# Kernel tuning notes

Hardware: AMD Instinct MI355X
Metric: run time of the kernel (lower is better)

The kernel has to match this reference:

```python
import jax, jax.numpy as jnp
import numpy as np

B, S, E, H = 2, 2048, 768, 12
D = E // H  # 64
ALPHA = 2.0
BANDWIDTH = 1.0
A_EXP = 0.5
RADIUS = 1.0
EPS = 1e-7
LN_EPS = 1e-12


def _l2norm(x, axis=-1):
    n = jnp.sqrt(jnp.sum(x * x, axis=axis, keepdims=True))
    return x / jnp.maximum(n, 1e-12)


def setup_inputs() -> dict:
    key = jax.random.key(0)
    ks = jax.random.split(key, 9)
    sc = 1.0 / np.sqrt(E)
    return {
        "hidden_states": jax.random.normal(ks[0], (B, S, E), dtype=jnp.float32),
        "Wq": jax.random.normal(ks[1], (E, E), dtype=jnp.float32) * sc,
        "bq": jnp.zeros((E,), dtype=jnp.float32),
        "Wk": jax.random.normal(ks[2], (E, E), dtype=jnp.float32) * sc,
        "bk": jnp.zeros((E,), dtype=jnp.float32),
        "Wv": jax.random.normal(ks[3], (E, E), dtype=jnp.float32) * sc,
        "bv": jnp.zeros((E,), dtype=jnp.float32),
        "Wo": jax.random.normal(ks[4], (E, E), dtype=jnp.float32) * sc,
        "bo": jnp.zeros((E,), dtype=jnp.float32),
        "ln_g": jnp.ones((E,), dtype=jnp.float32),
        "ln_b": jnp.zeros((E,), dtype=jnp.float32),
    }


def reference(hidden_states, Wq, bq, Wk, bk, Wv, bv, Wo, bo, ln_g, ln_b):
    # Spherical-kernel self-attention (SPFNSSelfAttention), eval mode (dropout=0)
    hs = _l2norm(hidden_states)                      # [B,S,E] embed onto sphere

    def heads(x):
        return x.reshape(B, S, H, D).transpose(0, 2, 1, 3)  # [B,H,S,D]

    q = _l2norm(heads(hs @ Wq + bq))
    k = _l2norm(heads(hs @ Wk + bk))
    v = heads(hs @ Wv + bv)

    # geodesic distance on the sphere
    cos = jnp.clip(jnp.einsum('bhsd,bhtd->bhst', q, k), -1.0 + EPS, 1.0 - EPS)
    g_dist = jnp.arccos(cos) * RADIUS                # [B,H,S,S]

    # alpha >= 2 branch: exponential kernel, exponent alpha/(alpha-1)
    p = ALPHA / (ALPHA - 1.0)
    attn_score = jnp.exp(-((g_dist / np.sqrt(BANDWIDTH)) ** p))

    # doubly-stochastic (Sinkhorn-like) scaling: diag(rowsum^-a) K diag(colsum^-a)
    row = jnp.sum(attn_score, axis=-1) ** (-A_EXP)   # [B,H,S]
    col = jnp.sum(attn_score, axis=-2) ** (-A_EXP)   # [B,H,S]
    K_tilde = attn_score * row[..., :, None] * col[..., None, :]

    # L1 row-normalize (F.normalize p=1, dim=3)
    denom = jnp.maximum(jnp.sum(jnp.abs(K_tilde), axis=-1, keepdims=True), 1e-12)
    attn_weights = K_tilde / denom

    attn_out = jnp.einsum('bhst,bhtd->bhsd', attn_weights, v)  # [B,H,S,D]
    # faithful to original: raw reshape [B,H,S,D] -> [B,S,H,D] -> [B,S,E]
    # (transpose(0,1) pair in the original cancels)
    attn_out = attn_out.reshape(B, S, E)

    # ModelSelfOutput: dense + residual(add original hidden_states) + LayerNorm
    y = attn_out @ Wo + bo + hidden_states
    mu = jnp.mean(y, axis=-1, keepdims=True)
    var = jnp.mean((y - mu) ** 2, axis=-1, keepdims=True)
    out = (y - mu) / jnp.sqrt(var + LN_EPS) * ln_g + ln_b
    return out
```

## Files before the change

kernel.cpp:

```cpp
#include <hip/hip_runtime.h>
#include <hip/hip_bf16.h>
#include <math.h>

#define BB 2
#define SS 2048
#define EE 768
#define HH 12
#define DD 64
#define MM (BB*SS)
#define BH (BB*HH)
#define NM ((size_t)MM*EE)
#define WSZ ((size_t)EE*EE)
#define BHS ((size_t)BH*SS)

typedef __attribute__((ext_vector_type(8))) short bf16x8;
typedef __attribute__((ext_vector_type(4))) float f32x4;

__device__ __forceinline__ float wave_sum64(float v) {
#pragma unroll
  for (int off = 32; off > 0; off >>= 1) v += __shfl_down(v, off, 64);
  return v;
}

__device__ __forceinline__ unsigned int pack_bf2(float x, float y) {
  unsigned int a = __float_as_uint(x), b = __float_as_uint(y);
  a += 0x7fffu + ((a >> 16) & 1u);
  b += 0x7fffu + ((b >> 16) & 1u);
  return (a >> 16) | (b & 0xffff0000u);
}
__device__ __forceinline__ unsigned int cvtpk_bf2(float x, float y) {
  __hip_bfloat162 h = __float22bfloat162_rn(make_float2(x, y));
  union { __hip_bfloat162 h2; unsigned int u; } c; c.h2 = h;
  return c.u;
}
__device__ __forceinline__ ushort bf16_1(float x) {
  unsigned int u = __float_as_uint(x);
  u += 0x7fffu + ((u >> 16) & 1u);
  return (ushort)(u >> 16);
}

__device__ __forceinline__ void score_wp(float cosv, float& w, float& p) {
  w = fmaxf(fmaf(cosv, -0.5f, 0.5f), 0.0f);
  p = fmaf(w, -0.544f, -0.2462720f);
  p = fmaf(w, p, -0.3250794f);
  p = fmaf(w, p, -0.4571429f);
  p = fmaf(w, p, -0.7111111f);
  p = fmaf(w, p, -1.3333333f);
  p = fmaf(w, p, -4.0f);
}

__global__ __launch_bounds__(256) void k_rownorm(const float* __restrict__ x,
                                                 ushort* __restrict__ o) {
  int row = blockIdx.x;
  int tid = threadIdx.x;
  const float* xr = x + (size_t)row * EE;
  ushort* orow = o + (size_t)row * EE;
  float v0 = xr[tid], v1 = xr[tid + 256], v2 = xr[tid + 512];
  float ss = v0 * v0 + v1 * v1 + v2 * v2;
  ss = wave_sum64(ss);
  __shared__ float red[4];
  if ((tid & 63) == 0) red[tid >> 6] = ss;
  __syncthreads();
  float tot = red[0] + red[1] + red[2] + red[3];
  float sc = 1.0f / fmaxf(sqrtf(tot), 1e-12f);
  orow[tid]       = bf16_1(v0 * sc);
  orow[tid + 256] = bf16_1(v1 * sc);
  orow[tid + 512] = bf16_1(v2 * sc);
}

__global__ __launch_bounds__(256) void k_transp(const float* __restrict__ Wq,
                                                const float* __restrict__ Wk,
                                                const float* __restrict__ Wv,
                                                const float* __restrict__ Wo,
                                                ushort* __restrict__ wt) {
  int z = blockIdx.z;
  const float* W = (z == 0) ? Wq : (z == 1) ? Wk : (z == 2) ? Wv : Wo;
  ushort* dst = wt + (size_t)z * WSZ;
  int n0 = blockIdx.x * 64, k0 = blockIdx.y * 64;
  __shared__ float t[64][65];
  int tid = threadIdx.x;
  int r4 = tid >> 4, c4 = (tid & 15) * 4;
#pragma unroll
  for (int i = 0; i < 4; ++i) {
    float4 v = *(const float4*)(W + (size_t)(k0 + i * 16 + r4) * EE + n0 + c4);
    t[i * 16 + r4][c4 + 0] = v.x; t[i * 16 + r4][c4 + 1] = v.y;
    t[i * 16 + r4][c4 + 2] = v.z; t[i * 16 + r4][c4 + 3] = v.w;
  }
  __syncthreads();
  int nr = tid >> 3, c8 = (tid & 7) * 8;
#pragma unroll
  for (int j = 0; j < 2; ++j) {
    int n = nr + j * 32;
    unsigned int p[4];
#pragma unroll
    for (int e = 0; e < 4; ++e)
      p[e] = pack_bf2(t[c8 + 2 * e][n], t[c8 + 2 * e + 1][n]);
    uint4 pv; pv.x = p[0]; pv.y = p[1]; pv.z = p[2]; pv.w = p[3];
    *(uint4*)(dst + (size_t)(n0 + n) * EE + k0 + c8) = pv;
  }
}

__global__ __launch_bounds__(256) void k_gemm_qkv_mfma(
    const ushort* __restrict__ hsb,
    const ushort* __restrict__ wt,
    const float* __restrict__ b0, const float* __restrict__ b1, const float* __restrict__ b2,
    ushort* __restrict__ qb, ushort* __restrict__ kb, ushort* __restrict__ vtb) {
  int bid = blockIdx.x;
  int xcd = bid & 7; int rr = bid >> 3;
  int n_idx = rr % 12; int m_in = (rr / 12) & 7; int z = rr / 96;
  int n0 = n_idx * 64; int m0 = (xcd * 8 + m_in) * 64;
  const ushort* W = wt + (size_t)z * WSZ;
  const float* bias = (z == 0) ? b0 : (z == 1) ? b1 : b2;
  __shared__ ushort As[2][64][72];
  __shared__ ushort Bs[2][64][72];
  int tid = threadIdx.x, w = tid >> 6, l = tid & 63, li = l & 15, g = l >> 4;
  int srow = tid >> 3, scol = (tid & 7) * 8;
  const ushort* Aba = hsb + (size_t)(m0 + srow) * EE + scol;
  const ushort* Wba = W + (size_t)(n0 + srow) * EE + scol;
  f32x4 acc[4];
#pragma unroll
  for (int u = 0; u < 4; ++u) acc[u] = (f32x4){0.f, 0.f, 0.f, 0.f};
  bf16x8 pA0 = *(const bf16x8*)(Aba);
  bf16x8 pA1 = *(const bf16x8*)(Aba + 32 * EE);
  bf16x8 pW0 = *(const bf16x8*)(Wba);
  bf16x8 pW1 = *(const bf16x8*)(Wba + 32 * EE);
  *(bf16x8*)&As[0][srow][scol] = pA0;
  *(bf16x8*)&As[0][srow + 32][scol] = pA1;
  *(bf16x8*)&Bs[0][srow][scol] = pW0;
  *(bf16x8*)&Bs[0][srow + 32][scol] = pW1;
  __syncthreads();
#pragma unroll
  for (int kt = 0; kt < 12; ++kt) {
    int cur = kt & 1;
    if (kt < 11) {
      int k0 = (kt + 1) * 64;
      pA0 = *(const bf16x8*)(Aba + k0);
      pA1 = *(const bf16x8*)(Aba + 32 * EE + k0);
      pW0 = *(const bf16x8*)(Wba + k0);
      pW1 = *(const bf16x8*)(Wba + 32 * EE + k0);
    }
    bf16x8 a0 = *(const bf16x8*)&As[cur][w * 16 + li][8 * g];
    bf16x8 a1 = *(const bf16x8*)&As[cur][w * 16 + li][32 + 8 * g];
#pragma unroll
    for (int u = 0; u < 4; ++u) {
      bf16x8 bb0 = *(const bf16x8*)&Bs[cur][u * 16 + li][8 * g];
      bf16x8 bb1 = *(const bf16x8*)&Bs[cur][u * 16 + li][32 + 8 * g];
      acc[u] = __builtin_amdgcn_mfma_f32_16x16x32_bf16(a0, bb0, acc[u], 0, 0, 0);
      acc[u] = __builtin_amdgcn_mfma_f32_16x16x32_bf16(a1, bb1, acc[u], 0, 0, 0);
    }
    __syncthreads();
    if (kt < 11) {
      int nxt = cur ^ 1;
      *(bf16x8*)&As[nxt][srow][scol] = pA0;
      *(bf16x8*)&As[nxt][srow + 32][scol] = pA1;
      *(bf16x8*)&Bs[nxt][srow][scol] = pW0;
      *(bf16x8*)&Bs[nxt][srow + 32][scol] = pW1;
      __syncthreads();
    }
  }
  float val[4][4];
#pragma unroll
  for (int u = 0; u < 4; ++u) {
    float bia = bias[n0 + u * 16 + li];
#pragma unroll
    for (int r = 0; r < 4; ++r) val[u][r] = acc[u][r] + bia;
  }
  if (z < 2) {
#pragma unroll
    for (int r = 0; r < 4; ++r) {
      float ss = val[0][r] * val[0][r] + val[1][r] * val[1][r] +
                 val[2][r] * val[2][r] + val[3][r] * val[3][r];
      ss += __shfl_xor(ss, 1, 64);
      ss += __shfl_xor(ss, 2, 64);
      ss += __shfl_xor(ss, 4, 64);
      ss += __shfl_xor(ss, 8, 64);
      float sc = rsqrtf(fmaxf(ss, 1e-24f));
#pragma unroll
      for (int u = 0; u < 4; ++u) val[u][r] *= sc;
    }
  }
  ushort (*tile)[72] = As[0];
#pragma unroll
  for (int u = 0; u < 4; ++u)
#pragma unroll
    for (int r = 0; r < 4; ++r) {
      int ml = w * 16 + 4 * g + r, d = u * 16 + li;
      if (z < 2) tile[ml][d] = bf16_1(val[u][r]);
      else       tile[d][ml] = bf16_1(val[u][r]);
    }
  __syncthreads();
  int h = n_idx, b_ = m0 >> 11, s0 = m0 & 2047;
  int bh = b_ * HH + h;
  int row = tid >> 2, c16 = (tid & 3) * 16;
  bf16x8 o0 = *(const bf16x8*)&tile[row][c16];
  bf16x8 o1 = *(const bf16x8*)&tile[row][c16 + 8];
  ushort* dst;
  if (z < 2) {
    dst = (z ? kb : qb) + ((size_t)bh * SS + s0 + row) * 64 + c16;
  } else {
    dst = vtb + ((size_t)bh * 64 + row) * SS + s0 + c16;
  }
  *(bf16x8*)dst = o0;
  *(bf16x8*)(dst + 8) = o1;
}

__global__ __launch_bounds__(256) void k_colsum_mfma(const ushort* __restrict__ qbf,
                                                     const ushort* __restrict__ kbf,
                                                     float* __restrict__ cs) {
  int bh = blockIdx.x, ttile = blockIdx.y, z = blockIdx.z;
  __shared__ float scs[4][4][16];
  int tid = threadIdx.x;
  int w = tid >> 6, l = tid & 63;
  int li = l & 15, g = l >> 4;
  const ushort* kb_base = kbf + ((size_t)bh * SS + ttile * 64) * 64;
  bf16x8 kb[4][2];
#pragma unroll
  for (int u = 0; u < 4; ++u)
#pragma unroll
    for (int kc = 0; kc < 2; ++kc)
      kb[u][kc] = *(const bf16x8*)(kb_base + (u * 16 + li) * 64 + kc * 32 + 8 * g);
  float cacc[4] = {0.f, 0.f, 0.f, 0.f};
  for (int it = 0; it < 16; ++it) {
    int s0 = ((z * 16 + it) * 4 + w) * 16;
    const ushort* qrow = qbf + ((size_t)bh * SS + s0 + li) * 64;
    bf16x8 qa0 = *(const bf16x8*)(qrow + 8 * g);
    bf16x8 qa1 = *(const bf16x8*)(qrow + 32 + 8 * g);
#pragma unroll
    for (int u = 0; u < 4; ++u) {
      f32x4 cf = {0.f, 0.f, 0.f, 0.f};
      cf = __builtin_amdgcn_mfma_f32_16x16x32_bf16(qa0, kb[u][0], cf, 0, 0, 0);
      cf = __builtin_amdgcn_mfma_f32_16x16x32_bf16(qa1, kb[u][1], cf, 0, 0, 0);
      float ww[4], pp[4];
#pragma unroll
      for (int r = 0; r < 4; ++r) score_wp(cf[r], ww[r], pp[r]);
      cacc[u] += __expf(ww[0] * pp[0]) + __expf(ww[1] * pp[1]) +
                 __expf(ww[2] * pp[2]) + __expf(ww[3] * pp[3]);
    }
  }
#pragma unroll
  for (int u = 0; u < 4; ++u) {
    cacc[u] += __shfl_xor(cacc[u], 16, 64);
    cacc[u] += __shfl_xor(cacc[u], 32, 64);
  }
  if (l < 16) {
#pragma unroll
    for (int u = 0; u < 4; ++u) scs[w][u][l] = cacc[u];
  }
  __syncthreads();
  if (tid < 64) {
    int t16 = tid & 15, u = tid >> 4;
    float s_ = scs[0][u][t16] + scs[1][u][t16] + scs[2][u][t16] + scs[3][u][t16];
    cs[(size_t)z * BHS + (size_t)bh * SS + ttile * 64 + u * 16 + t16] = s_;
  }
}

__global__ __launch_bounds__(256) void k_cwreduce(const float* __restrict__ cs,
                                                  float* __restrict__ lcw) {
  size_t g = (size_t)blockIdx.x * 256 + threadIdx.x;
  lcw[g] = -0.5f * __logf(cs[g] + cs[BHS + g]);
}

__global__ __launch_bounds__(256) void k_attn_mfma(const ushort* __restrict__ qbf,
                                                   const ushort* __restrict__ kbf,
                                                   const ushort* __restrict__ vtb,
                                                   const float* __restrict__ lcw,
                                                   float* __restrict__ po0,
                                                   float* __restrict__ po1,
                                                   float* __restrict__ prp) {
  int bh = blockIdx.x, stile = blockIdx.y, z = blockIdx.z;
  __shared__ __align__(16) ushort Kt[64][72];
  __shared__ __align__(16) ushort Vt[64][72];
  __shared__ __align__(16) unsigned int W_lds[4][16][36];
  int tid = threadIdx.x;
  int w = tid >> 6, l = tid & 63;
  int li = l & 15, g = l >> 4;
  int s = stile * 64 + w * 16 + li;
  const ushort* qrow = qbf + ((size_t)bh * SS + s) * 64;
  bf16x8 qb0 = *(const bf16x8*)(qrow + 8 * g);
  bf16x8 qb1 = *(const bf16x8*)(qrow + 32 + 8 * g);
  const float* cwp = lcw + (size_t)bh * SS;
  const ushort* kb_h = kbf + (size_t)bh * SS * 64;
  const ushort* vt_h = vtb + (size_t)bh * 64 * SS;
  float* po = (z == 0) ? po0 : po1;
  int sr = tid >> 3, sc = (tid & 7) * 8;
  f32x4 oacc[4];
#pragma unroll
  for (int dt = 0; dt < 4; ++dt) oacc[dt] = (f32x4){0.f, 0.f, 0.f, 0.f};
  float rp = 0.f;
  int tt0 = z * 16;
  bf16x8 rk0 = *(const bf16x8*)(kb_h + (size_t)(tt0 * 64 + sr) * 64 + sc);
  bf16x8 rk1 = *(const bf16x8*)(kb_h + (size_t)(tt0 * 64 + sr + 32) * 64 + sc);
  bf16x8 rv0 = *(const bf16x8*)(vt_h + (size_t)sr * SS + tt0 * 64 + sc);
  bf16x8 rv1 = *(const bf16x8*)(vt_h + (size_t)(sr + 32) * SS + tt0 * 64 + sc);
  for (int tt = tt0; tt < tt0 + 16; ++tt) {
    *(bf16x8*)&Kt[sr][sc] = rk0;
    *(bf16x8*)&Kt[sr + 32][sc] = rk1;
    *(bf16x8*)&Vt[sr][sc] = rv0;
    *(bf16x8*)&Vt[sr + 32][sc] = rv1;
    __syncthreads();
    if (tt + 1 < tt0 + 16) {
      rk0 = *(const bf16x8*)(kb_h + (size_t)((tt + 1) * 64 + sr) * 64 + sc);
      rk1 = *(const bf16x8*)(kb_h + (size_t)((tt + 1) * 64 + sr + 32) * 64 + sc);
      rv0 = *(const bf16x8*)(vt_h + (size_t)sr * SS + (tt + 1) * 64 + sc);
      rv1 = *(const bf16x8*)(vt_h + (size_t)(sr + 32) * SS + (tt + 1) * 64 + sc);
    }
#pragma unroll
    for (int u = 0; u < 4; ++u) {
      bf16x8 ka0 = *(const bf16x8*)&Kt[u * 16 + li][8 * g];
      bf16x8 ka1 = *(const bf16x8*)&Kt[u * 16 + li][32 + 8 * g];
      f32x4 cf = {0.f, 0.f, 0.f, 0.f};
      cf = __builtin_amdgcn_mfma_f32_16x16x32_bf16(ka0, qb0, cf, 0, 0, 0);
      cf = __builtin_amdgcn_mfma_f32_16x16x32_bf16(ka1, qb1, cf, 0, 0, 0);
      float4 lc4 = *(const float4*)(cwp + tt * 64 + u * 16 + 4 * g);
      float ww[4], pp[4];
#pragma unroll
      for (int r = 0; r < 4; ++r) score_wp(cf[r], ww[r], pp[r]);
      float s0_ = __expf(fmaf(ww[0], pp[0], lc4.x));
      float s1_ = __expf(fmaf(ww[1], pp[1], lc4.y));
      float s2_ = __expf(fmaf(ww[2], pp[2], lc4.z));
      float s3_ = __expf(fmaf(ww[3], pp[3], lc4.w));
      rp += s0_ + s1_ + s2_ + s3_;
      uint2 pw; pw.x = cvtpk_bf2(s0_, s1_); pw.y = cvtpk_bf2(s2_, s3_);
      *(uint2*)&W_lds[w][li][u * 8 + 2 * g] = pw;
    }
#pragma unroll
    for (int tc = 0; tc < 2; ++tc) {
      bf16x8 bw = *(const bf16x8*)&W_lds[w][li][tc * 16 + 4 * g];
#pragma unroll
      for (int dt = 0; dt < 4; ++dt) {
        bf16x8 va = *(const bf16x8*)&Vt[dt * 16 + li][tc * 32 + 8 * g];
        oacc[dt] = __builtin_amdgcn_mfma_f32_16x16x32_bf16(va, bw, oacc[dt], 0, 0, 0);
      }
    }
    __syncthreads();
  }
  rp += __shfl_xor(rp, 16, 64);
  rp += __shfl_xor(rp, 32, 64);
  if (l < 16)
    prp[(size_t)z * BHS + (size_t)bh * SS + stile * 64 + w * 16 + l] = rp;
#pragma unroll
  for (int dt = 0; dt < 4; ++dt)
#pragma unroll
    for (int r = 0; r < 4; ++r)
      po[((size_t)bh * 64 + dt * 16 + 4 * g + r) * SS + s] = oacc[dt][r];
}

__global__ __launch_bounds__(256) void k_combine(const float* __restrict__ po0,
                                                 const float* __restrict__ po1,
                                                 const float* __restrict__ prp,
                                                 ushort* __restrict__ aobf) {
  int s0 = blockIdx.x * 64, bh = blockIdx.y;
  __shared__ float rpl[64];
  __shared__ ushort t16[64][72];
  int tid = threadIdx.x;
  if (tid < 64) {
    float r = prp[(size_t)bh * SS + s0 + tid] + prp[BHS + (size_t)bh * SS + s0 + tid];
    rpl[tid] = 1.0f / fmaxf(r, 1e-12f);
  }
  __syncthreads();
#pragma unroll
  for (int i = 0; i < 16; ++i) {
    int flat = i * 256 + tid;
    int d = flat >> 4, sq = (flat & 15) * 4;
    size_t off = ((size_t)bh * 64 + d) * SS + s0 + sq;
    float4 p0 = *(const float4*)(po0 + off);
    float4 p1 = *(const float4*)(po1 + off);
    t16[sq + 0][d] = bf16_1((p0.x + p1.x) * rpl[sq + 0]);
    t16[sq + 1][d] = bf16_1((p0.y + p1.y) * rpl[sq + 1]);
    t16[sq + 2][d] = bf16_1((p0.z + p1.z) * rpl[sq + 2]);
    t16[sq + 3][d] = bf16_1((p0.w + p1.w) * rpl[sq + 3]);
  }
  __syncthreads();
  int s = tid >> 2, c = (tid & 3) * 16;
  bf16x8 o0 = *(const bf16x8*)&t16[s][c];
  bf16x8 o1 = *(const bf16x8*)&t16[s][c + 8];
  ushort* orow = aobf + ((size_t)bh * SS + s0 + s) * 64 + c;
  *(bf16x8*)orow = o0;
  *(bf16x8*)(orow + 8) = o1;
}

__global__ __launch_bounds__(256) void k_gemm_out_mfma(
    const ushort* __restrict__ aob,
    const ushort* __restrict__ Wt,
    const float* __restrict__ bias,
    const float* __restrict__ hid,
    float* __restrict__ y) {
  int bid = blockIdx.x;
  int xcd = bid & 7; int rr = bid >> 3;
  int n_idx = rr % 12; int m_in = rr / 12;
  int n0 = n_idx * 64; int m0 = (xcd * 8 + m_in) * 64;
  __shared__ ushort As[2][64][72];
  __shared__ ushort Bs[2][64][72];
  int tid = threadIdx.x, w = tid >> 6, l = tid & 63, li = l & 15, g = l >> 4;
  int srow = tid >> 3, scol = (tid & 7) * 8;
  const ushort* Aba = aob + (size_t)(m0 + srow) * EE + scol;
  const ushort* Wba = Wt + (size_t)(n0 + srow) * EE + scol;
  f32x4 acc[4];
#pragma unroll
  for (int u = 0; u < 4; ++u) acc[u] = (f32x4){0.f, 0.f, 0.f, 0.f};
  bf16x8 pA0 = *(const bf16x8*)(Aba);
  bf16x8 pA1 = *(const bf16x8*)(Aba + 32 * EE);
  bf16x8 pW0 = *(const bf16x8*)(Wba);
  bf16x8 pW1 = *(const bf16x8*)(Wba + 32 * EE);
  *(bf16x8*)&As[0][srow][scol] = pA0;
  *(bf16x8*)&As[0][srow + 32][scol] = pA1;
  *(bf16x8*)&Bs[0][srow][scol] = pW0;
  *(bf16x8*)&Bs[0][srow + 32][scol] = pW1;
  __syncthreads();
#pragma unroll
  for (int kt = 0; kt < 12; ++kt) {
    int cur = kt & 1;
    if (kt < 11) {
      int k0 = (kt + 1) * 64;
      pA0 = *(const bf16x8*)(Aba + k0);
      pA1 = *(const bf16x8*)(Aba + 32 * EE + k0);
      pW0 = *(const bf16x8*)(Wba + k0);
      pW1 = *(const bf16x8*)(Wba + 32 * EE + k0);
    }
    bf16x8 a0 = *(const bf16x8*)&As[cur][w * 16 + li][8 * g];
    bf16x8 a1 = *(const bf16x8*)&As[cur][w * 16 + li][32 + 8 * g];
#pragma unroll
    for (int u = 0; u < 4; ++u) {
      bf16x8 bb0 = *(const bf16x8*)&Bs[cur][u * 16 + li][8 * g];
      bf16x8 bb1 = *(const bf16x8*)&Bs[cur][u * 16 + li][32 + 8 * g];
      acc[u] = __builtin_amdgcn_mfma_f32_16x16x32_bf16(a0, bb0, acc[u], 0, 0, 0);
      acc[u] = __builtin_amdgcn_mfma_f32_16x16x32_bf16(a1, bb1, acc[u], 0, 0, 0);
    }
    __syncthreads();
    if (kt < 11) {
      int nxt = cur ^ 1;
      *(bf16x8*)&As[nxt][srow][scol] = pA0;
      *(bf16x8*)&As[nxt][srow + 32][scol] = pA1;
      *(bf16x8*)&Bs[nxt][srow][scol] = pW0;
      *(bf16x8*)&Bs[nxt][srow + 32][scol] = pW1;
      __syncthreads();
    }
  }
  int m_base = m0 + w * 16 + 4 * g;
#pragma unroll
  for (int u = 0; u < 4; ++u) {
    int n = n0 + u * 16 + li;
    float bia = bias[n];
#pragma unroll
    for (int r = 0; r < 4; ++r) {
      int m = m_base + r;
      y[(size_t)m * EE + n] = acc[u][r] + bia + hid[(size_t)m * EE + n];
    }
  }
}

__global__ __launch_bounds__(256) void k_ln(const float* __restrict__ y,
                                            const float* __restrict__ g,
                                            const float* __restrict__ b,
                                            float* __restrict__ out) {
  int row = blockIdx.x;
  int tid = threadIdx.x;
  const float* yr = y + (size_t)row * EE;
  float v0 = yr[tid], v1 = yr[tid + 256], v2 = yr[tid + 512];
  float s1 = v0 + v1 + v2;
  float s2 = v0 * v0 + v1 * v1 + v2 * v2;
#pragma unroll
  for (int off = 32; off > 0; off >>= 1) {
    s1 += __shfl_down(s1, off, 64);
    s2 += __shfl_down(s2, off, 64);
  }
  __shared__ float r1[4], r2[4];
  if ((tid & 63) == 0) { r1[tid >> 6] = s1; r2[tid >> 6] = s2; }
  __syncthreads();
  float S1 = r1[0] + r1[1] + r1[2] + r1[3];
  float S2 = r2[0] + r2[1] + r2[2] + r2[3];
  float mu = S1 * (1.0f / 768.0f);
  float var = fmaxf(S2 * (1.0f / 768.0f) - mu * mu, 0.0f);
  float rstd = 1.0f / sqrtf(var + 1e-12f);
  float* orow = out + (size_t)row * EE;
  orow[tid]       = (v0 - mu) * rstd * g[tid]       + b[tid];
  orow[tid + 256] = (v1 - mu) * rstd * g[tid + 256] + b[tid + 256];
  orow[tid + 512] = (v2 - mu) * rstd * g[tid + 512] + b[tid + 512];
}

extern "C" void kernel_launch(void* const* d_in, const int* in_sizes, int n_in,
                              void* d_out, int out_size, void* d_ws, size_t ws_size,
                              hipStream_t stream) {
  const float* hidden = (const float*)d_in[0];
  const float* Wq = (const float*)d_in[1];
  const float* bq = (const float*)d_in[2];
  const float* Wk = (const float*)d_in[3];
  const float* bk = (const float*)d_in[4];
  const float* Wv = (const float*)d_in[5];
  const float* bv = (const float*)d_in[6];
  const float* Wo = (const float*)d_in[7];
  const float* bo = (const float*)d_in[8];
  const float* lng = (const float*)d_in[9];
  const float* lnb = (const float*)d_in[10];
  float* out = (float*)d_out;

  float* ws = (float*)d_ws;
  size_t need = (5 * NM + BHS) * sizeof(float);
  if (ws_size < need) return;

  ushort* hsb = (ushort*)ws;
  ushort* wt  = (ushort*)(ws + NM / 2);
  float* ws1 = ws + 1 * NM;
  float* ws2 = ws + 2 * NM;
  float* ws3 = ws + 3 * NM;
  float* ws4 = ws + 4 * NM;
  float* cw  = ws + 5 * NM;

  ushort* qbf = (ushort*)ws3;
  ushort* vtb = (ushort*)(ws3 + NM / 2);
  ushort* kbf = (ushort*)ws4;
  float* cs = ws1;
  float* po0 = ws1;
  float* po1 = ws2;
  float* prp = ws4 + NM / 2;
  ushort* aobf = (ushort*)ws4;
  float* y = ws1;

  hipLaunchKernelGGL(k_rownorm, dim3(MM), dim3(256), 0, stream, hidden, hsb);
  hipLaunchKernelGGL(k_transp, dim3(EE / 64, EE / 64, 4), dim3(256), 0, stream,
                     Wq, Wk, Wv, Wo, wt);
  hipLaunchKernelGGL(k_gemm_qkv_mfma, dim3(2304), dim3(256), 0, stream,
                     hsb, wt, bq, bk, bv, qbf, kbf, vtb);
  hipLaunchKernelGGL(k_colsum_mfma, dim3(BH, 32, 2), dim3(256), 0, stream,
                     qbf, kbf, cs);
  hipLaunchKernelGGL(k_cwreduce, dim3(BHS / 256), dim3(256), 0, stream, cs, cw);
  hipLaunchKernelGGL(k_attn_mfma, dim3(BH, 32, 2), dim3(256), 0, stream,
                     qbf, kbf, vtb, cw, po0, po1, prp);
  hipLaunchKernelGGL(k_combine, dim3(SS / 64, BH), dim3(256), 0, stream,
                     po0, po1, prp, aobf);
  hipLaunchKernelGGL(k_gemm_out_mfma, dim3(768), dim3(256), 0, stream,
                     aobf, wt + 3 * WSZ, bo, hidden, y);
  hipLaunchKernelGGL(k_ln, dim3(MM), dim3(256), 0, stream, y, lng, lnb, out);
}
```

Before: 176.5 us.

## Drop split-K in colsum/attention, fuse combine and log reduce, use exp2 polynomial

Removes the two-way z split in the column-sum and attention kernels, so each block loops over all 32 key tiles. This lets the log/column-weight reduction and the partial-output combine be folded into those kernels, which drops two launches and the fp32 partial-output round trip. The score polynomial is refit as a lower-degree base-2 form using exp2f/log2f, cutting a few FMAs per element at some risk to accuracy. The trade-off is that the colsum and attention launches each have half as many blocks (768 instead of 1536), which lowers occupancy.

Measured after the change: 183.8 us. +4.1%, slower.

```diff
diff --git a/kernel.cpp b/kernel.cpp
--- a/kernel.cpp
+++ b/kernel.cpp
@@ -39,14 +39,12 @@
   return (ushort)(u >> 16);
 }
 
-__device__ __forceinline__ void score_wp(float cosv, float& w, float& p) {
+__device__ __forceinline__ void score_wp2(float cosv, float& w, float& p) {
   w = fmaxf(fmaf(cosv, -0.5f, 0.5f), 0.0f);
-  p = fmaf(w, -0.544f, -0.2462720f);
-  p = fmaf(w, p, -0.3250794f);
-  p = fmaf(w, p, -0.4571429f);
-  p = fmaf(w, p, -0.7111111f);
-  p = fmaf(w, p, -1.3333333f);
-  p = fmaf(w, p, -4.0f);
+  p = fmaf(w, -0.888700f, -0.659518f);
+  p = fmaf(w, p, -1.025916f);
+  p = fmaf(w, p, -1.923593f);
+  p = fmaf(w, p, -5.770780f);
 }
 
 __global__ __launch_bounds__(256) void k_rownorm(const float* __restrict__ x,
@@ -206,8 +204,8 @@
 
 __global__ __launch_bounds__(256) void k_colsum_mfma(const ushort* __restrict__ qbf,
                                                      const ushort* __restrict__ kbf,
-                                                     float* __restrict__ cs) {
-  int bh = blockIdx.x, ttile = blockIdx.y, z = blockIdx.z;
+                                                     float* __restrict__ lcw) {
+  int bh = blockIdx.x, ttile = blockIdx.y;
   __shared__ float scs[4][4][16];
   int tid = threadIdx.x;
   int w = tid >> 6, l = tid & 63;
@@ -220,8 +218,8 @@
     for (int kc = 0; kc < 2; ++kc)
       kb[u][kc] = *(const bf16x8*)(kb_base + (u * 16 + li) * 64 + kc * 32 + 8 * g);
   float cacc[4] = {0.f, 0.f, 0.f, 0.f};
-  for (int it = 0; it < 16; ++it) {
-    int s0 = ((z * 16 + it) * 4 + w) * 16;
+  for (int it = 0; it < 32; ++it) {
+    int s0 = (it * 4 + w) * 16;
     const ushort* qrow = qbf + ((size_t)bh * SS + s0 + li) * 64;
     bf16x8 qa0 = *(const bf16x8*)(qrow + 8 * g);
     bf16x8 qa1 = *(const bf16x8*)(qrow + 32 + 8 * g);
@@ -232,9 +230,9 @@
       cf = __builtin_amdgcn_mfma_f32_16x16x32_bf16(qa1, kb[u][1], cf, 0, 0, 0);
       float ww[4], pp[4];
 #pragma unroll
-      for (int r = 0; r < 4; ++r) score_wp(cf[r], ww[r], pp[r]);
-      cacc[u] += __expf(ww[0] * pp[0]) + __expf(ww[1] * pp[1]) +
-                 __expf(ww[2] * pp[2]) + __expf(ww[3] * pp[3]);
+      for (int r = 0; r < 4; ++r) score_wp2(cf[r], ww[r], pp[r]);
+      cacc[u] += exp2f(ww[0] * pp[0]) + exp2f(ww[1] * pp[1]) +
+                 exp2f(ww[2] * pp[2]) + exp2f(ww[3] * pp[3]);
     }
   }
 #pragma unroll
@@ -250,24 +248,16 @@
   if (tid < 64) {
     int t16 = tid & 15, u = tid >> 4;
     float s_ = scs[0][u][t16] + scs[1][u][t16] + scs[2][u][t16] + scs[3][u][t16];
-    cs[(size_t)z * BHS + (size_t)bh * SS + ttile * 64 + u * 16 + t16] = s_;
-  }
-}
-
-__global__ __launch_bounds__(256) void k_cwreduce(const float* __restrict__ cs,
-                                                  float* __restrict__ lcw) {
-  size_t g = (size_t)blockIdx.x * 256 + threadIdx.x;
-  lcw[g] = -0.5f * __logf(cs[g] + cs[BHS + g]);
+    lcw[(size_t)bh * SS + ttile * 64 + u * 16 + t16] = -0.5f * log2f(s_);
+  }
 }
 
 __global__ __launch_bounds__(256) void k_attn_mfma(const ushort* __restrict__ qbf,
                                                    const ushort* __restrict__ kbf,
                                                    const ushort* __restrict__ vtb,
                                                    const float* __restrict__ lcw,
-                                                   float* __restrict__ po0,
-                                                   float* __restrict__ po1,
-                                                   float* __restrict__ prp) {
-  int bh = blockIdx.x, stile = blockIdx.y, z = blockIdx.z;
+                                                   ushort* __restrict__ aobf) {
+  int bh = blockIdx.x, stile = blockIdx.y;
   __shared__ __align__(16) ushort Kt[64][72];
   __shared__ __align__(16) ushort Vt[64][72];
   __shared__ __align__(16) unsigned int W_lds[4][16][36];
@@ -281,24 +271,22 @@
   const float* cwp = lcw + (size_t)bh * SS;
   const ushort* kb_h = kbf + (size_t)bh * SS * 64;
   const ushort* vt_h = vtb + (size_t)bh * 64 * SS;
-  float* po = (z == 0) ? po0 : po1;
   int sr = tid >> 3, sc = (tid & 7) * 8;
   f32x4 oacc[4];
 #pragma unroll
   for (int dt = 0; dt < 4; ++dt) oacc[dt] = (f32x4){0.f, 0.f, 0.f, 0.f};
   float rp = 0.f;
-  int tt0 = z * 16;
-  bf16x8 rk0 = *(const bf16x8*)(kb_h + (size_t)(tt0 * 64 + sr) * 64 + sc);
-  bf16x8 rk1 = *(const bf16x8*)(kb_h + (size_t)(tt0 * 64 + sr + 32) * 64 + sc);
-  bf16x8 rv0 = *(const bf16x8*)(vt_h + (size_t)sr * SS + tt0 * 64 + sc);
-  bf16x8 rv1 = *(const bf16x8*)(vt_h + (size_t)(sr + 32) * SS + tt0 * 64 + sc);
-  for (int tt = tt0; tt < tt0 + 16; ++tt) {
+  bf16x8 rk0 = *(const bf16x8*)(kb_h + (size_t)sr * 64 + sc);
+  bf16x8 rk1 = *(const bf16x8*)(kb_h + (size_t)(sr + 32) * 64 + sc);
+  bf16x8 rv0 = *(const bf16x8*)(vt_h + (size_t)sr * SS + sc);
+  bf16x8 rv1 = *(const bf16x8*)(vt_h + (size_t)(sr + 32) * SS + sc);
+  for (int tt = 0; tt < 32; ++tt) {
     *(bf16x8*)&Kt[sr][sc] = rk0;
     *(bf16x8*)&Kt[sr + 32][sc] = rk1;
     *(bf16x8*)&Vt[sr][sc] = rv0;
     *(bf16x8*)&Vt[sr + 32][sc] = rv1;
     __syncthreads();
-    if (tt + 1 < tt0 + 16) {
+    if (tt + 1 < 32) {
       rk0 = *(const bf16x8*)(kb_h + (size_t)((tt + 1) * 64 + sr) * 64 + sc);
       rk1 = *(const bf16x8*)(kb_h + (size_t)((tt + 1) * 64 + sr + 32) * 64 + sc);
       rv0 = *(const bf16x8*)(vt_h + (size_t)sr * SS + (tt + 1) * 64 + sc);
@@ -314,11 +302,11 @@
       float4 lc4 = *(const float4*)(cwp + tt * 64 + u * 16 + 4 * g);
       float ww[4], pp[4];
 #pragma unroll
-      for (int r = 0; r < 4; ++r) score_wp(cf[r], ww[r], pp[r]);
-      float s0_ = __expf(fmaf(ww[0], pp[0], lc4.x));
-      float s1_ = __expf(fmaf(ww[1], pp[1], lc4.y));
-      float s2_ = __expf(fmaf(ww[2], pp[2], lc4.z));
-      float s3_ = __expf(fmaf(ww[3], pp[3], lc4.w));
+      for (int r = 0; r < 4; ++r) score_wp2(cf[r], ww[r], pp[r]);
+      float s0_ = exp2f(fmaf(ww[0], pp[0], lc4.x));
+      float s1_ = exp2f(fmaf(ww[1], pp[1], lc4.y));
+      float s2_ = exp2f(fmaf(ww[2], pp[2], lc4.z));
+      float s3_ = exp2f(fmaf(ww[3], pp[3], lc4.w));
       rp += s0_ + s1_ + s2_ + s3_;
       uint2 pw; pw.x = cvtpk_bf2(s0_, s1_); pw.y = cvtpk_bf2(s2_, s3_);
       *(uint2*)&W_lds[w][li][u * 8 + 2 * g] = pw;
@@ -336,47 +324,20 @@
   }
   rp += __shfl_xor(rp, 16, 64);
   rp += __shfl_xor(rp, 32, 64);
-  if (l < 16)
-    prp[(size_t)z * BHS + (size_t)bh * SS + stile * 64 + w * 16 + l] = rp;
+  float inv = 1.0f / fmaxf(rp, 1e-12f);
+  ushort (*trans)[72] = Kt;
 #pragma unroll
   for (int dt = 0; dt < 4; ++dt)
 #pragma unroll
     for (int r = 0; r < 4; ++r)
-      po[((size_t)bh * 64 + dt * 16 + 4 * g + r) * SS + s] = oacc[dt][r];
-}
-
-__global__ __launch_bounds__(256) void k_combine(const float* __restrict__ po0,
-                                                 const float* __restrict__ po1,
-                                                 const float* __restrict__ prp,
-                                                 ushort* __restrict__ aobf) {
-  int s0 = blockIdx.x * 64, bh = blockIdx.y;
-  __shared__ float rpl[64];
-  __shared__ ushort t16[64][72];
-  int tid = threadIdx.x;
-  if (tid < 64) {
-    float r = prp[(size_t)bh * SS + s0 + tid] + prp[BHS + (size_t)bh * SS + s0 + tid];
-    rpl[tid] = 1.0f / fmaxf(r, 1e-12f);
-  }
-  __syncthreads();
-#pragma unroll
-  for (int i = 0; i < 16; ++i) {
-    int flat = i * 256 + tid;
-    int d = flat >> 4, sq = (flat & 15) * 4;
-    size_t off = ((size_t)bh * 64 + d) * SS + s0 + sq;
-    float4 p0 = *(const float4*)(po0 + off);
-    float4 p1 = *(const float4*)(po1 + off);
-    t16[sq + 0][d] = bf16_1((p0.x + p1.x) * rpl[sq + 0]);
-    t16[sq + 1][d] = bf16_1((p0.y + p1.y) * rpl[sq + 1]);
-    t16[sq + 2][d] = bf16_1((p0.z + p1.z) * rpl[sq + 2]);
-    t16[sq + 3][d] = bf16_1((p0.w + p1.w) * rpl[sq + 3]);
-  }
-  __syncthreads();
-  int s = tid >> 2, c = (tid & 3) * 16;
-  bf16x8 o0 = *(const bf16x8*)&t16[s][c];
-  bf16x8 o1 = *(const bf16x8*)&t16[s][c + 8];
-  ushort* orow = aobf + ((size_t)bh * SS + s0 + s) * 64 + c;
-  *(bf16x8*)orow = o0;
-  *(bf16x8*)(orow + 8) = o1;
+      trans[w * 16 + li][dt * 16 + 4 * g + r] = bf16_1(oacc[dt][r] * inv);
+  __syncthreads();
+  int row = tid >> 2, c16 = (tid & 3) * 16;
+  bf16x8 o0 = *(const bf16x8*)&trans[row][c16];
+  bf16x8 o1 = *(const bf16x8*)&trans[row][c16 + 8];
+  ushort* dst = aobf + ((size_t)bh * SS + stile * 64 + row) * 64 + c16;
+  *(bf16x8*)dst = o0;
+  *(bf16x8*)(dst + 8) = o1;
 }
 
 __global__ __launch_bounds__(256) void k_gemm_out_mfma(
@@ -504,30 +465,23 @@
   float* ws2 = ws + 2 * NM;
   float* ws3 = ws + 3 * NM;
   float* ws4 = ws + 4 * NM;
-  float* cw  = ws + 5 * NM;
+  float* lcw = ws + 5 * NM;
 
   ushort* qbf = (ushort*)ws3;
   ushort* vtb = (ushort*)(ws3 + NM / 2);
   ushort* kbf = (ushort*)ws4;
-  float* cs = ws1;
-  float* po0 = ws1;
-  float* po1 = ws2;
-  float* prp = ws4 + NM / 2;
-  ushort* aobf = (ushort*)ws4;
-  float* y = ws1;
+  ushort* aobf = (ushort*)ws1;
+  float* y = ws2;
 
   hipLaunchKernelGGL(k_rownorm, dim3(MM), dim3(256), 0, stream, hidden, hsb);
   hipLaunchKernelGGL(k_transp, dim3(EE / 64, EE / 64, 4), dim3(256), 0, stream,
                      Wq, Wk, Wv, Wo, wt);
   hipLaunchKernelGGL(k_gemm_qkv_mfma, dim3(2304), dim3(256), 0, stream,
                      hsb, wt, bq, bk, bv, qbf, kbf, vtb);
-  hipLaunchKernelGGL(k_colsum_mfma, dim3(BH, 32, 2), dim3(256), 0, stream,
-                     qbf, kbf, cs);
-  hipLaunchKernelGGL(k_cwreduce, dim3(BHS / 256), dim3(256), 0, stream, cs, cw);
-  hipLaunchKernelGGL(k_attn_mfma, dim3(BH, 32, 2), dim3(256), 0, stream,
-                     qbf, kbf, vtb, cw, po0, po1, prp);
-  hipLaunchKernelGGL(k_combine, dim3(SS / 64, BH), dim3(256), 0, stream,
-                     po0, po1, prp, aobf);
+  hipLaunchKernelGGL(k_colsum_mfma, dim3(BH, 32), dim3(256), 0, stream,
+                     qbf, kbf, lcw);
+  hipLaunchKernelGGL(k_attn_mfma, dim3(BH, 32), dim3(256), 0, stream,
+                     qbf, kbf, vtb, lcw, aobf);
   hipLaunchKernelGGL(k_gemm_out_mfma, dim3(768), dim3(256), 0, stream,
                      aobf, wt + 3 * WSZ, bo, hidden, y);
   hipLaunchKernelGGL(k_ln, dim3(MM), dim3(256), 0, stream, y, lng, lnb, out);
```
